# Kernel optimization log

Measured on AMD Instinct MI355X. Metric: run time of the kernel, lower is better.

## Reference

```python
import jax, jax.numpy as jnp
import numpy as np

P = 256      # identities
K = 16       # instances per identity per modality
C = 4096     # feature dim
MARGIN = 0.6 # margin_euc


def setup_inputs() -> dict:
    key = jax.random.key(0)
    x = jax.random.normal(key, (2 * P * K, C), dtype=jnp.float32)
    half = jnp.repeat(jnp.arange(P, dtype=jnp.int64), K)
    pids = jnp.concatenate([half, half])
    return {"x": x, "pids": pids}


def reference(x, pids):
    n = x.shape[0]          # 2*P*K
    twop = 2 * P
    # hierarchy-center features: mean over the K instances of each (modality, id) group
    pidhc = pids.reshape(twop, -1)[:, 0]                    # [2P]
    hcen = x.reshape(twop, -1, C).mean(axis=1)              # [2P, C]
    # euclidean distance matrix [N, 2P]
    d2 = ((x * x).sum(axis=1, keepdims=True)
          + (hcen * hcen).sum(axis=1)[None, :]
          - 2.0 * (x @ hcen.T))
    dist = jnp.sqrt(jnp.clip(d2, 1e-12))
    mask = pids[:, None] == pidhc[None, :]                  # same-identity mask

    # loss1: cross-modal positive pull. Rows in first half (modality 0) match
    # centers in second column half (modality 1 centers), and vice versa.
    row_first = (jnp.arange(n) < n // 2)[:, None]           # [N,1]
    col_second = (jnp.arange(twop) >= P)[None, :]           # [1,2P]
    sel = mask & (row_first == col_second)
    loss1 = jnp.sum(jnp.where(sel, dist, 0.0)) / jnp.sum(sel).astype(dist.dtype)

    # loss2: margin push on all non-matching centers
    neg = ~mask
    hinge = jnp.maximum(MARGIN - dist, 0.0)
    loss2 = jnp.sum(jnp.where(neg, hinge, 0.0)) / jnp.sum(neg).astype(dist.dtype)

    return loss1 + loss2
```

## Files before the change

kernel.cpp:

```cpp
#include <hip/hip_runtime.h>
#include <math.h>

#define P_    256
#define K_    16
#define C_    4096
#define C4_   1024
#define N_    8192
#define TWOP  512
#define NSL   16
#define W4    64
#define NTAILB 32
#define MARGIN_F 0.6f
#define EXCAP   8192
#define FLAGCAP 16384

__device__ __forceinline__ float wave_reduce_f(float v) {
    #pragma unroll
    for (int o = 32; o > 0; o >>= 1) v += __shfl_xor(v, o, 64);
    return v;
}

__global__ __launch_bounds__(256) void k_fused(const float* __restrict__ x,
                                               float* __restrict__ dot_part,
                                               float* __restrict__ sq_part,
                                               float* __restrict__ hn2_part,
                                               unsigned* __restrict__ counters) {
    const int blk = blockIdx.x;
    const int p = blk >> 4;
    const int s = blk & (NSL - 1);
    const int t = threadIdx.x;
    const int lane = t & 63;
    const int wv = t >> 6;

    if (blk == 0 && t < 3) counters[t] = 0u;

    __shared__ float4 partA[4][W4];
    __shared__ float4 partB[4][W4];
    __shared__ float4 shA[W4];
    __shared__ float4 shB[W4];

    const float4* x4 = (const float4*)x;
    const int col = s * W4 + lane;

    float4 v[8];
    #pragma unroll
    for (int q = 0; q < 8; ++q) {
        const int r = q * 4 + wv;
        const int grp = (r < 16) ? p : (P_ + p);
        v[q] = x4[((size_t)grp * K_ + (r & 15)) * C4_ + col];
    }
    float4 sA = {0.f,0.f,0.f,0.f}, sB = {0.f,0.f,0.f,0.f};
    #pragma unroll
    for (int q = 0; q < 4; ++q) { sA.x += v[q].x; sA.y += v[q].y; sA.z += v[q].z; sA.w += v[q].w; }
    #pragma unroll
    for (int q = 4; q < 8; ++q) { sB.x += v[q].x; sB.y += v[q].y; sB.z += v[q].z; sB.w += v[q].w; }
    partA[wv][lane] = sA;
    partB[wv][lane] = sB;
    __syncthreads();

    if (wv < 2) {
        float4 a;
        if (wv == 0) {
            float4 u0 = partA[0][lane], u1 = partA[1][lane], u2 = partA[2][lane], u3 = partA[3][lane];
            a.x = (u0.x+u1.x+u2.x+u3.x) * 0.0625f;
            a.y = (u0.y+u1.y+u2.y+u3.y) * 0.0625f;
            a.z = (u0.z+u1.z+u2.z+u3.z) * 0.0625f;
            a.w = (u0.w+u1.w+u2.w+u3.w) * 0.0625f;
            shA[lane] = a;
        } else {
            float4 u0 = partB[0][lane], u1 = partB[1][lane], u2 = partB[2][lane], u3 = partB[3][lane];
            a.x = (u0.x+u1.x+u2.x+u3.x) * 0.0625f;
            a.y = (u0.y+u1.y+u2.y+u3.y) * 0.0625f;
            a.z = (u0.z+u1.z+u2.z+u3.z) * 0.0625f;
            a.w = (u0.w+u1.w+u2.w+u3.w) * 0.0625f;
            shB[lane] = a;
        }
        float hn = a.x*a.x + a.y*a.y + a.z*a.z + a.w*a.w;
        hn = wave_reduce_f(hn);
        if (lane == 0) hn2_part[(p * NSL + s) * 2 + wv] = hn;
    }
    __syncthreads();

    const float4 hA = shA[lane];
    const float4 hB = shB[lane];
    const int outbase = (p * NSL + s) * 32;
    #pragma unroll
    for (int q = 0; q < 8; ++q) {
        const float4 a = v[q];
        const float4 h = (q < 4) ? hB : hA;
        float dp = a.x*h.x + a.y*h.y + a.z*h.z + a.w*h.w;
        float sq = a.x*a.x + a.y*a.y + a.z*a.z + a.w*a.w;
        #pragma unroll
        for (int o = 32; o > 0; o >>= 1) {
            dp += __shfl_xor(dp, o, 64);
            sq += __shfl_xor(sq, o, 64);
        }
        if (lane == 0) {
            dot_part[outbase + q*4 + wv] = dp;
            sq_part [outbase + q*4 + wv] = sq;
        }
    }
}

__global__ __launch_bounds__(256) void k_tail(const float* __restrict__ dot_part,
                                              const float* __restrict__ sq_part,
                                              const float* __restrict__ hn2_part,
                                              const int* __restrict__ pids,
                                              float* __restrict__ xn,
                                              float* __restrict__ hng2,
                                              float* __restrict__ s1part,
                                              unsigned* __restrict__ c1part,
                                              unsigned* __restrict__ negpart,
                                              unsigned* __restrict__ counters,
                                              int* __restrict__ extralist,
                                              int* __restrict__ flaglist) {
    __shared__ int   gp[TWOP];
    __shared__ float shn[TWOP];
    __shared__ float sh2[TWOP];
    __shared__ int   s_ok;
    __shared__ float s_min[4], s_max[4];
    __shared__ float rf[4];
    __shared__ unsigned ru[4], rn[4];
    const int t = threadIdx.x;
    const int lane = t & 63, wv = t >> 6;

    if (t == 0) s_ok = 1;
    __syncthreads();

    float lmin = 3.0e38f, lmax = -3.0e38f;
    for (int j = t; j < TWOP; j += 256) {
        const int g = pids[j * K_];
        gp[j] = g;
        if (g != (j & (P_ - 1))) s_ok = 0;
        const int side = (j < P_) ? 0 : 1;
        const int pp = j & (P_ - 1);
        float a = 0.f;
        #pragma unroll
        for (int s = 0; s < NSL; ++s) a += hn2_part[(pp * NSL + s) * 2 + side];
        sh2[j] = a;
        const float r = sqrtf(a);
        shn[j] = r;
        lmin = fminf(lmin, r); lmax = fmaxf(lmax, r);
    }
    #pragma unroll
    for (int o = 32; o > 0; o >>= 1) {
        lmin = fminf(lmin, __shfl_xor(lmin, o, 64));
        lmax = fmaxf(lmax, __shfl_xor(lmax, o, 64));
    }
    if (lane == 0) { s_min[wv] = lmin; s_max[wv] = lmax; }
    __syncthreads();
    const float hmin = fminf(fminf(s_min[0], s_min[1]), fminf(s_min[2], s_min[3]));
    const float hmax = fmaxf(fmaxf(s_max[0], s_max[1]), fmaxf(s_max[2], s_max[3]));
    const int structured = s_ok;

    if (blockIdx.x == 0)
        for (int j = t; j < TWOP; j += 256) hng2[j] = sh2[j];

    const int gr  = blockIdx.x * 256 + t;
    const int grp = gr >> 4, kk = gr & 15;
    const int p   = grp & (P_ - 1);
    const int r   = (grp < P_) ? kk : 16 + kk;
    const int pg  = (grp < P_) ? (P_ + p) : p;

    float dot = 0.f, sq = 0.f;
    #pragma unroll
    for (int s = 0; s < NSL; ++s) {
        dot += dot_part[(p * NSL + s) * 32 + r];
        sq  += sq_part [(p * NSL + s) * 32 + r];
    }
    const float dist = sqrtf(fmaxf(sq + sh2[pg] - 2.0f * dot, 1e-12f));
    const float myxn = sqrtf(sq);
    xn[gr] = myxn;

    const int mypid = pids[gr];
    const bool window_clear = (myxn >= hmax + MARGIN_F) || (myxn <= hmin - MARGIN_F);

    unsigned mall, mopp;
    if (structured && mypid == p && window_clear) {
        mall = 2u; mopp = 1u;
    } else {
        const int jb = (gr < N_ / 2) ? P_ : 0;
        mall = 0u; mopp = 0u;
        for (int j = 0; j < TWOP; ++j) {
            if (gp[j] == mypid) {
                ++mall;
                if (j >= jb && j < jb + P_) {
                    ++mopp;
                    if (j != pg) {
                        unsigned s0 = atomicAdd(&counters[0], 1u);
                        if (s0 < EXCAP) extralist[s0] = gr * TWOP + j;
                        else atomicExch(&counters[2], 1u);
                    }
                }
            } else {
                if (fabsf(myxn - shn[j]) < MARGIN_F) {
                    unsigned s0 = atomicAdd(&counters[1], 1u);
                    if (s0 < FLAGCAP) flaglist[s0] = gr * TWOP + j;
                    else atomicExch(&counters[2], 1u);
                }
            }
        }
    }

    float s1 = (gp[pg] == mypid) ? dist : 0.f;
    unsigned neg = (unsigned)TWOP - mall;
    unsigned mo = mopp;
    #pragma unroll
    for (int o = 32; o > 0; o >>= 1) {
        s1  += __shfl_xor(s1, o, 64);
        mo  += __shfl_xor(mo, o, 64);
        neg += __shfl_xor(neg, o, 64);
    }
    if (lane == 0) { rf[wv] = s1; ru[wv] = mo; rn[wv] = neg; }
    __syncthreads();
    if (t == 0) {
        s1part[blockIdx.x]  = rf[0] + rf[1] + rf[2] + rf[3];
        c1part[blockIdx.x]  = ru[0] + ru[1] + ru[2] + ru[3];
        negpart[blockIdx.x] = rn[0] + rn[1] + rn[2] + rn[3];
    }
}

__global__ __launch_bounds__(256) void k_final(const float* __restrict__ x,
                                               const float* __restrict__ xn,
                                               const float* __restrict__ hng2,
                                               const float* __restrict__ s1part,
                                               const unsigned* __restrict__ c1part,
                                               const unsigned* __restrict__ negpart,
                                               const unsigned* __restrict__ counters,
                                               const int* __restrict__ extralist,
                                               const int* __restrict__ flaglist,
                                               float* __restrict__ out) {
    const int t = threadIdx.x;
    const int lane = t & 63;
    __shared__ float red[4];
    __shared__ float sS1, sC1, sNG;

    {
        float s1 = 0.f; unsigned c1 = 0u, ng = 0u;
        if (t < NTAILB) { s1 = s1part[t]; c1 = c1part[t]; ng = negpart[t]; }
        if (t < 64) {
            #pragma unroll
            for (int o = 32; o > 0; o >>= 1) {
                s1 += __shfl_xor(s1, o, 64);
                c1 += __shfl_xor(c1, o, 64);
                ng += __shfl_xor(ng, o, 64);
            }
            if (t == 0) { sS1 = s1; sC1 = (float)c1; sNG = (float)ng; }
        }
    }
    __syncthreads();

    unsigned ne = counters[0]; if (ne > EXCAP)   ne = EXCAP;
    unsigned nf = counters[1]; if (nf > FLAGCAP) nf = FLAGCAP;
    float s1x = 0.f, l2 = 0.f;
    const float4* x4 = (const float4*)x;
    for (unsigned u = 0; u < ne + nf; ++u) {
        const bool isex = (u < ne);
        const int code = isex ? extralist[u] : flaglist[u - ne];
        const int i = code >> 9, jj = code & (TWOP - 1);
        const float4* xr = x4 + (size_t)i * C4_;
        const float4* gb = x4 + (size_t)jj * K_ * C4_;
        float dp = 0.f;
        for (int c = t; c < C4_; c += 256) {
            const float4 a = xr[c];
            float4 hs = {0.f,0.f,0.f,0.f};
            #pragma unroll
            for (int rr = 0; rr < K_; ++rr) {
                const float4 u4 = gb[(size_t)rr * C4_ + c];
                hs.x += u4.x; hs.y += u4.y; hs.z += u4.z; hs.w += u4.w;
            }
            dp += a.x*hs.x + a.y*hs.y + a.z*hs.z + a.w*hs.w;
        }
        dp *= 0.0625f;
        dp = wave_reduce_f(dp);
        if (lane == 0) red[t >> 6] = dp;
        __syncthreads();
        if (t == 0) {
            const float ddot = red[0] + red[1] + red[2] + red[3];
            const float d2 = xn[i]*xn[i] + hng2[jj] - 2.0f * ddot;
            const float dist = sqrtf(fmaxf(d2, 1e-12f));
            if (isex) s1x += dist;
            else { const float h = MARGIN_F - dist; if (h > 0.f) l2 += h; }
        }
        __syncthreads();
    }

    if (t == 0) out[0] = (sS1 + s1x) / sC1 + l2 / sNG;
}

extern "C" void kernel_launch(void* const* d_in, const int* in_sizes, int n_in,
                              void* d_out, int out_size, void* d_ws, size_t ws_size,
                              hipStream_t stream) {
    const float* x    = (const float*)d_in[0];
    const int*   pids = (const int*)d_in[1];

    float* ws = (float*)d_ws;
    float*    dot_part = ws;
    float*    sq_part  = dot_part + P_ * NSL * 32;
    float*    hn2_part = sq_part + P_ * NSL * 32;
    float*    xn       = hn2_part + P_ * NSL * 2;
    float*    hng2     = xn + N_;
    float*    s1part   = hng2 + TWOP;
    unsigned* c1part   = (unsigned*)(s1part + NTAILB);
    unsigned* negpart  = c1part + NTAILB;
    unsigned* counters = negpart + NTAILB;
    int*      extralist= (int*)(counters + 3);
    int*      flaglist = extralist + EXCAP;

    hipLaunchKernelGGL(k_fused, dim3(P_ * NSL), dim3(256), 0, stream,
                       x, dot_part, sq_part, hn2_part, counters);
    hipLaunchKernelGGL(k_tail,  dim3(NTAILB),   dim3(256), 0, stream,
                       dot_part, sq_part, hn2_part, pids, xn, hng2,
                       s1part, c1part, negpart, counters, extralist, flaglist);
    hipLaunchKernelGGL(k_final, dim3(1),        dim3(256), 0, stream,
                       x, xn, hng2, s1part, c1part, negpart, counters,
                       extralist, flaglist, (float*)d_out);
}
```

Baseline: 39.93 us.

## Fold final kernel into tail via last-block counter, use transposed butterfly reduction

```diff
diff --git a/kernel.cpp b/kernel.cpp
--- a/kernel.cpp
+++ b/kernel.cpp
@@ -3,7 +3,6 @@
 
 #define P_    256
 #define K_    16
-#define C_    4096
 #define C4_   1024
 #define N_    8192
 #define TWOP  512
@@ -32,7 +31,7 @@
     const int lane = t & 63;
     const int wv = t >> 6;
 
-    if (blk == 0 && t < 3) counters[t] = 0u;
+    if (blk == 0 && t < 4) counters[t] = 0u;
 
     __shared__ float4 partA[4][W4];
     __shared__ float4 partB[4][W4];
@@ -59,22 +58,15 @@
     __syncthreads();
 
     if (wv < 2) {
+        const float4* Pp = (wv == 0) ? &partA[0][0] : &partB[0][0];
+        const float4 u0 = Pp[0*W4 + lane], u1 = Pp[1*W4 + lane];
+        const float4 u2 = Pp[2*W4 + lane], u3 = Pp[3*W4 + lane];
         float4 a;
-        if (wv == 0) {
-            float4 u0 = partA[0][lane], u1 = partA[1][lane], u2 = partA[2][lane], u3 = partA[3][lane];
-            a.x = (u0.x+u1.x+u2.x+u3.x) * 0.0625f;
-            a.y = (u0.y+u1.y+u2.y+u3.y) * 0.0625f;
-            a.z = (u0.z+u1.z+u2.z+u3.z) * 0.0625f;
-            a.w = (u0.w+u1.w+u2.w+u3.w) * 0.0625f;
-            shA[lane] = a;
-        } else {
-            float4 u0 = partB[0][lane], u1 = partB[1][lane], u2 = partB[2][lane], u3 = partB[3][lane];
-            a.x = (u0.x+u1.x+u2.x+u3.x) * 0.0625f;
-            a.y = (u0.y+u1.y+u2.y+u3.y) * 0.0625f;
-            a.z = (u0.z+u1.z+u2.z+u3.z) * 0.0625f;
-            a.w = (u0.w+u1.w+u2.w+u3.w) * 0.0625f;
-            shB[lane] = a;
-        }
+        a.x = (u0.x+u1.x+u2.x+u3.x) * 0.0625f;
+        a.y = (u0.y+u1.y+u2.y+u3.y) * 0.0625f;
+        a.z = (u0.z+u1.z+u2.z+u3.z) * 0.0625f;
+        a.w = (u0.w+u1.w+u2.w+u3.w) * 0.0625f;
+        if (wv == 0) shA[lane] = a; else shB[lane] = a;
         float hn = a.x*a.x + a.y*a.y + a.z*a.z + a.w*a.w;
         hn = wave_reduce_f(hn);
         if (lane == 0) hn2_part[(p * NSL + s) * 2 + wv] = hn;
@@ -83,44 +75,62 @@
 
     const float4 hA = shA[lane];
     const float4 hB = shB[lane];
-    const int outbase = (p * NSL + s) * 32;
+
+    float val[16];
     #pragma unroll
     for (int q = 0; q < 8; ++q) {
         const float4 a = v[q];
         const float4 h = (q < 4) ? hB : hA;
-        float dp = a.x*h.x + a.y*h.y + a.z*h.z + a.w*h.w;
-        float sq = a.x*a.x + a.y*a.y + a.z*a.z + a.w*a.w;
-        #pragma unroll
-        for (int o = 32; o > 0; o >>= 1) {
-            dp += __shfl_xor(dp, o, 64);
-            sq += __shfl_xor(sq, o, 64);
-        }
-        if (lane == 0) {
-            dot_part[outbase + q*4 + wv] = dp;
-            sq_part [outbase + q*4 + wv] = sq;
-        }
+        val[q]     = a.x*h.x + a.y*h.y + a.z*h.z + a.w*h.w;
+        val[8 + q] = a.x*a.x + a.y*a.y + a.z*a.z + a.w*a.w;
+    }
+
+    #define BFLY_STAGE(MASK, HALF)                                          \
+    {                                                                       \
+        const bool upper = (lane & MASK) != 0;                              \
+        _Pragma("unroll")                                                   \
+        for (int i = 0; i < HALF; ++i) {                                    \
+            const float send = upper ? val[i] : val[i + HALF];              \
+            const float recv = __shfl_xor(send, MASK, 64);                  \
+            val[i] = (upper ? val[i + HALF] : val[i]) + recv;               \
+        }                                                                   \
+    }
+    BFLY_STAGE(1, 8)
+    BFLY_STAGE(2, 4)
+    BFLY_STAGE(4, 2)
+    BFLY_STAGE(8, 1)
+    #undef BFLY_STAGE
+    val[0] += __shfl_xor(val[0], 16, 64);
+    val[0] += __shfl_xor(val[0], 32, 64);
+
+    if (lane < 16) {
+        const int idx = ((lane & 1) << 3) | ((lane & 2) << 1)
+                      | ((lane & 4) >> 1) | ((lane & 8) >> 3);
+        const int outbase = (p * NSL + s) * 32;
+        if (idx < 8) dot_part[outbase + idx * 4 + wv] = val[0];
+        else         sq_part [outbase + (idx - 8) * 4 + wv] = val[0];
     }
 }
 
-__global__ __launch_bounds__(256) void k_tail(const float* __restrict__ dot_part,
+__global__ __launch_bounds__(256) void k_tail(const float* __restrict__ x,
+                                              const float* __restrict__ dot_part,
                                               const float* __restrict__ sq_part,
                                               const float* __restrict__ hn2_part,
                                               const int* __restrict__ pids,
-                                              float* __restrict__ xn,
-                                              float* __restrict__ hng2,
                                               float* __restrict__ s1part,
                                               unsigned* __restrict__ c1part,
                                               unsigned* __restrict__ negpart,
                                               unsigned* __restrict__ counters,
                                               int* __restrict__ extralist,
-                                              int* __restrict__ flaglist) {
+                                              int* __restrict__ flaglist,
+                                              float* __restrict__ out) {
     __shared__ int   gp[TWOP];
-    __shared__ float shn[TWOP];
-    __shared__ float sh2[TWOP];
-    __shared__ int   s_ok;
-    __shared__ float s_min[4], s_max[4];
+    __shared__ float shn[TWOP], sh2[TWOP];
+    __shared__ int   s_ok, sLast;
+    __shared__ float smin[4], smax[4];
     __shared__ float rf[4];
     __shared__ unsigned ru[4], rn[4];
+    __shared__ float bc_s1, bc_c1, bc_ng;
     const int t = threadIdx.x;
     const int lane = t & 63, wv = t >> 6;
 
@@ -147,14 +157,11 @@
         lmin = fminf(lmin, __shfl_xor(lmin, o, 64));
         lmax = fmaxf(lmax, __shfl_xor(lmax, o, 64));
     }
-    if (lane == 0) { s_min[wv] = lmin; s_max[wv] = lmax; }
-    __syncthreads();
-    const float hmin = fminf(fminf(s_min[0], s_min[1]), fminf(s_min[2], s_min[3]));
-    const float hmax = fmaxf(fmaxf(s_max[0], s_max[1]), fmaxf(s_max[2], s_max[3]));
+    if (lane == 0) { smin[wv] = lmin; smax[wv] = lmax; }
+    __syncthreads();
+    const float hmin = fminf(fminf(smin[0], smin[1]), fminf(smin[2], smin[3]));
+    const float hmax = fmaxf(fmaxf(smax[0], smax[1]), fmaxf(smax[2], smax[3]));
     const int structured = s_ok;
-
-    if (blockIdx.x == 0)
-        for (int j = t; j < TWOP; j += 256) hng2[j] = sh2[j];
 
     const int gr  = blockIdx.x * 256 + t;
     const int grp = gr >> 4, kk = gr & 15;
@@ -170,8 +177,6 @@
     }
     const float dist = sqrtf(fmaxf(sq + sh2[pg] - 2.0f * dot, 1e-12f));
     const float myxn = sqrtf(sq);
-    xn[gr] = myxn;
-
     const int mypid = pids[gr];
     const bool window_clear = (myxn >= hmax + MARGIN_F) || (myxn <= hmin - MARGIN_F);
 
@@ -192,12 +197,10 @@
                         else atomicExch(&counters[2], 1u);
                     }
                 }
-            } else {
-                if (fabsf(myxn - shn[j]) < MARGIN_F) {
-                    unsigned s0 = atomicAdd(&counters[1], 1u);
-                    if (s0 < FLAGCAP) flaglist[s0] = gr * TWOP + j;
-                    else atomicExch(&counters[2], 1u);
-                }
+            } else if (fabsf(myxn - shn[j]) < MARGIN_F) {
+                unsigned s0 = atomicAdd(&counters[1], 1u);
+                if (s0 < FLAGCAP) flaglist[s0] = gr * TWOP + j;
+                else atomicExch(&counters[2], 1u);
             }
         }
     }
@@ -214,38 +217,31 @@
     if (lane == 0) { rf[wv] = s1; ru[wv] = mo; rn[wv] = neg; }
     __syncthreads();
     if (t == 0) {
-        s1part[blockIdx.x]  = rf[0] + rf[1] + rf[2] + rf[3];
-        c1part[blockIdx.x]  = ru[0] + ru[1] + ru[2] + ru[3];
-        negpart[blockIdx.x] = rn[0] + rn[1] + rn[2] + rn[3];
-    }
-}
-
-__global__ __launch_bounds__(256) void k_final(const float* __restrict__ x,
-                                               const float* __restrict__ xn,
-                                               const float* __restrict__ hng2,
-                                               const float* __restrict__ s1part,
-                                               const unsigned* __restrict__ c1part,
-                                               const unsigned* __restrict__ negpart,
-                                               const unsigned* __restrict__ counters,
-                                               const int* __restrict__ extralist,
-                                               const int* __restrict__ flaglist,
-                                               float* __restrict__ out) {
-    const int t = threadIdx.x;
-    const int lane = t & 63;
-    __shared__ float red[4];
-    __shared__ float sS1, sC1, sNG;
+        atomicExch(&s1part[blockIdx.x],  rf[0] + rf[1] + rf[2] + rf[3]);
+        atomicExch(&c1part[blockIdx.x],  ru[0] + ru[1] + ru[2] + ru[3]);
+        atomicExch(&negpart[blockIdx.x], rn[0] + rn[1] + rn[2] + rn[3]);
+    }
+
+    __threadfence();
+    if (t == 0) {
+        const unsigned n = atomicAdd(&counters[3], 1u);
+        sLast = (n == NTAILB - 1) ? 1 : 0;
+    }
+    __syncthreads();
+    if (!sLast) return;
+    __threadfence();
 
     {
-        float s1 = 0.f; unsigned c1 = 0u, ng = 0u;
-        if (t < NTAILB) { s1 = s1part[t]; c1 = c1part[t]; ng = negpart[t]; }
+        float s1v = 0.f; unsigned c1v = 0u, ngv = 0u;
+        if (t < NTAILB) { s1v = s1part[t]; c1v = c1part[t]; ngv = negpart[t]; }
         if (t < 64) {
             #pragma unroll
             for (int o = 32; o > 0; o >>= 1) {
-                s1 += __shfl_xor(s1, o, 64);
-                c1 += __shfl_xor(c1, o, 64);
-                ng += __shfl_xor(ng, o, 64);
+                s1v += __shfl_xor(s1v, o, 64);
+                c1v += __shfl_xor(c1v, o, 64);
+                ngv += __shfl_xor(ngv, o, 64);
             }
-            if (t == 0) { sS1 = s1; sC1 = (float)c1; sNG = (float)ng; }
+            if (t == 0) { bc_s1 = s1v; bc_c1 = (float)c1v; bc_ng = (float)ngv; }
         }
     }
     __syncthreads();
@@ -260,32 +256,37 @@
         const int i = code >> 9, jj = code & (TWOP - 1);
         const float4* xr = x4 + (size_t)i * C4_;
         const float4* gb = x4 + (size_t)jj * K_ * C4_;
-        float dp = 0.f;
+        float dp = 0.f, sqi = 0.f;
         for (int c = t; c < C4_; c += 256) {
             const float4 a = xr[c];
-            float4 hs = {0.f,0.f,0.f,0.f};
+            float hx = 0.f, hy = 0.f, hz = 0.f, hw = 0.f;
             #pragma unroll
             for (int rr = 0; rr < K_; ++rr) {
                 const float4 u4 = gb[(size_t)rr * C4_ + c];
-                hs.x += u4.x; hs.y += u4.y; hs.z += u4.z; hs.w += u4.w;
+                hx += u4.x; hy += u4.y; hz += u4.z; hw += u4.w;
             }
-            dp += a.x*hs.x + a.y*hs.y + a.z*hs.z + a.w*hs.w;
-        }
-        dp *= 0.0625f;
-        dp = wave_reduce_f(dp);
-        if (lane == 0) red[t >> 6] = dp;
+            dp  += (a.x*hx + a.y*hy + a.z*hz + a.w*hw) * 0.0625f;
+            sqi += a.x*a.x + a.y*a.y + a.z*a.z + a.w*a.w;
+        }
+        #pragma unroll
+        for (int o = 32; o > 0; o >>= 1) {
+            dp  += __shfl_xor(dp, o, 64);
+            sqi += __shfl_xor(sqi, o, 64);
+        }
+        if (lane == 0) { rf[wv] = dp; smin[wv] = sqi; }
         __syncthreads();
         if (t == 0) {
-            const float ddot = red[0] + red[1] + red[2] + red[3];
-            const float d2 = xn[i]*xn[i] + hng2[jj] - 2.0f * ddot;
-            const float dist = sqrtf(fmaxf(d2, 1e-12f));
-            if (isex) s1x += dist;
-            else { const float h = MARGIN_F - dist; if (h > 0.f) l2 += h; }
+            const float ddot = rf[0] + rf[1] + rf[2] + rf[3];
+            const float sqv  = smin[0] + smin[1] + smin[2] + smin[3];
+            const float d2 = sqv + sh2[jj] - 2.0f * ddot;
+            const float dist2 = sqrtf(fmaxf(d2, 1e-12f));
+            if (isex) s1x += dist2;
+            else { const float h = MARGIN_F - dist2; if (h > 0.f) l2 += h; }
         }
         __syncthreads();
     }
 
-    if (t == 0) out[0] = (sS1 + s1x) / sC1 + l2 / sNG;
+    if (t == 0) out[0] = (bc_s1 + s1x) / bc_c1 + l2 / bc_ng;
 }
 
 extern "C" void kernel_launch(void* const* d_in, const int* in_sizes, int n_in,
@@ -298,21 +299,17 @@
     float*    dot_part = ws;
     float*    sq_part  = dot_part + P_ * NSL * 32;
     float*    hn2_part = sq_part + P_ * NSL * 32;
-    float*    xn       = hn2_part + P_ * NSL * 2;
-    float*    hng2     = xn + N_;
-    float*    s1part   = hng2 + TWOP;
+    float*    s1part   = hn2_part + P_ * NSL * 2;
     unsigned* c1part   = (unsigned*)(s1part + NTAILB);
     unsigned* negpart  = c1part + NTAILB;
     unsigned* counters = negpart + NTAILB;
-    int*      extralist= (int*)(counters + 3);
+    int*      extralist= (int*)(counters + 4);
     int*      flaglist = extralist + EXCAP;
 
     hipLaunchKernelGGL(k_fused, dim3(P_ * NSL), dim3(256), 0, stream,
                        x, dot_part, sq_part, hn2_part, counters);
     hipLaunchKernelGGL(k_tail,  dim3(NTAILB),   dim3(256), 0, stream,
-                       dot_part, sq_part, hn2_part, pids, xn, hng2,
-                       s1part, c1part, negpart, counters, extralist, flaglist);
-    hipLaunchKernelGGL(k_final, dim3(1),        dim3(256), 0, stream,
-                       x, xn, hng2, s1part, c1part, negpart, counters,
+                       x, dot_part, sq_part, hn2_part, pids,
+                       s1part, c1part, negpart, counters,
                        extralist, flaglist, (float*)d_out);
 }
```

Result: faster. 37.59 us (-5.9%).
